# Optimization experiments

Measured on AMD Instinct MI355X. Metric: run time of the kernel, lower is better.

Reference implementation:

```python
import jax, jax.numpy as jnp
import numpy as np

B, H, W, C, HID, V, EMB = 16, 24, 96, 1024, 256, 5000, 256
BN_EPS = 1e-5


def _lin(k, fin, fout, s=0.05):
    return jax.random.normal(k, (fin, fout), jnp.float32) * s


def setup_inputs():
    ks = jax.random.split(jax.random.key(0), 24)
    inp = {
        "input_y": jax.random.randint(ks[0], (B,), 0, V),
        "input_hidden": jax.random.normal(ks[1], (B, 1, HID), jnp.float32),
        "img_feature": jax.random.normal(ks[2], (B, C, H, W), jnp.float32),
        "feature_w": W,
        "attention_sum": jnp.zeros((B, 1, H, W), jnp.float32),
        "alpha_t": jax.random.uniform(ks[3], (B, 1, H, W), jnp.float32),
        "feature_h": H,
        "batch_size": B,
        "h_mask": jax.random.randint(ks[4], (B,), 1, H + 1),
        "w_mask": jax.random.randint(ks[5], (B,), 1, W + 1),
        "emb_table": jax.random.normal(ks[6], (V, EMB), jnp.float32) * 0.05,
        "gru1_wi": _lin(ks[7], EMB, 3 * HID), "gru1_wh": _lin(ks[8], HID, 3 * HID),
        "gru1_bi": jnp.zeros((3 * HID,), jnp.float32), "gru1_bh": jnp.zeros((3 * HID,), jnp.float32),
        "fc1_w": _lin(ks[9], HID, 256), "fc1_b": jnp.zeros((256,), jnp.float32),
        "gru2_wi": _lin(ks[10], C, 3 * HID), "gru2_wh": _lin(ks[11], HID, 3 * HID),
        "gru2_bi": jnp.zeros((3 * HID,), jnp.float32), "gru2_bh": jnp.zeros((3 * HID,), jnp.float32),
        "out_w": _lin(ks[12], 128, V), "out_b": jnp.zeros((V,), jnp.float32),
        "emb2_w": _lin(ks[13], 256, 128), "emb2_b": jnp.zeros((128,), jnp.float32),
        "conv1_w": jax.random.normal(ks[14], (1, 1, 3, 3), jnp.float32) * 0.05,
        "conv1_b": jnp.zeros((1,), jnp.float32),
        "conv_tan_w": jax.random.normal(ks[15], (256, 256, 3, 3), jnp.float32) * 0.02,
        "conv_tan_b": jnp.zeros((256,), jnp.float32),
        "fc2_w": _lin(ks[16], HID, 128), "fc2_b": jnp.zeros((128,), jnp.float32),
        "ua_w": _lin(ks[17], C, 256), "ua_b": jnp.zeros((256,), jnp.float32),
        "uf_w": _lin(ks[18], 1, 256), "uf_b": jnp.zeros((256,), jnp.float32),
        "v_w": _lin(ks[19], 256, 1), "v_b": jnp.zeros((1,), jnp.float32),
        "wc_w": _lin(ks[20], C, 128), "wc_b": jnp.zeros((128,), jnp.float32),
        "bn1_gamma": jnp.ones((256,), jnp.float32), "bn1_beta": jnp.zeros((256,), jnp.float32),
        "bn1_mean": jnp.zeros((256,), jnp.float32), "bn1_var": jnp.ones((256,), jnp.float32),
    }
    return inp


def _gru(x, h, wi, wh, bi, bh):
    # PyTorch GRUCell semantics
    gi = x @ wi + bi
    gh = h @ wh + bh
    ir, iz, inn = jnp.split(gi, 3, axis=-1)
    hr, hz, hn = jnp.split(gh, 3, axis=-1)
    r = jax.nn.sigmoid(ir + hr)
    z = jax.nn.sigmoid(iz + hz)
    n = jnp.tanh(inn + r * hn)
    return (1.0 - z) * n + z * h


def _conv(x, w, b):
    y = jax.lax.conv_general_dilated(x, w, (1, 1), 'SAME',
                                     dimension_numbers=('NCHW', 'OIHW', 'NCHW'))
    return y + b[None, :, None, None]


def reference(input_y, input_hidden, img_feature, feature_w, attention_sum, alpha_t,
              feature_h, batch_size, h_mask, w_mask,
              emb_table, gru1_wi, gru1_wh, gru1_bi, gru1_bh, fc1_w, fc1_b,
              gru2_wi, gru2_wh, gru2_bi, gru2_bh, out_w, out_b, emb2_w, emb2_b,
              conv1_w, conv1_b, conv_tan_w, conv_tan_b, fc2_w, fc2_b,
              ua_w, ua_b, uf_w, uf_b, v_w, v_b, wc_w, wc_b,
              bn1_gamma, bn1_beta, bn1_mean, bn1_var):
    b, c, h, w = img_feature.shape
    # per-sample validity mask over the feature map  [B, H, W]
    et_mask = ((jnp.arange(h)[None, :] < h_mask[:, None])[:, :, None]
               & (jnp.arange(w)[None, :] < w_mask[:, None])[:, None, :]).astype(jnp.float32)

    emb = emb_table[input_y]                      # [B, 256] (dropout = identity, eval)
    h0 = input_hidden[:, 0, :]                    # [B, HID]
    st1 = _gru(emb, h0, gru1_wi, gru1_wh, gru1_bi, gru1_bh)
    st1 = st1 @ fc1_w + fc1_b                     # [B, 256]

    alpha_c = _conv(alpha_t, conv1_w, conv1_b)    # [B, 1, H, W]
    att_sum = attention_sum + alpha_c             # coverage accumulator

    img1 = jnp.einsum('bchw,cd->bhwd', img_feature, ua_w) + ua_b  # [B,H,W,256]
    att1 = att_sum[:, 0, :, :, None] * uf_w[0] + uf_b             # Linear(1,256)
    et = st1[:, None, None, :] + img1 + att1      # [B, H, W, 256]

    et_nchw = jnp.transpose(et, (0, 3, 1, 2))
    et_nchw = _conv(et_nchw, conv_tan_w, conv_tan_b)
    et_nchw = et_nchw * et_mask[:, None]
    inv = bn1_gamma / jnp.sqrt(bn1_var + BN_EPS)  # eval-mode BatchNorm2d(256)
    et_nchw = (et_nchw - bn1_mean[None, :, None, None]) * inv[None, :, None, None] \
              + bn1_beta[None, :, None, None]
    et_nchw = jnp.tanh(et_nchw)

    e = jnp.einsum('bchw,c->bhw', et_nchw, v_w[:, 0]) + v_b[0]    # [B, H, W]
    e_exp = jnp.exp(e) * et_mask
    e_sum = jnp.sum(e_exp, axis=(1, 2))
    alpha = e_exp / (e_sum[:, None, None] + 1e-8)                 # masked softmax

    ct = jnp.einsum('bhw,bchw->bc', alpha, img_feature)           # [B, 1024]
    st = _gru(ct, st1, gru2_wi, gru2_wh, gru2_bi, gru2_bh)        # [B, HID]
    hidden_next = st[:, None, :]

    pre = (st @ fc2_w + fc2_b) + (emb @ emb2_w + emb2_b) + (ct @ wc_w + wc_b)  # [B,128]
    output = jax.nn.log_softmax(pre @ out_w + out_b, axis=1)[:, None, :]       # [B,1,V]
    return output, hidden_next, alpha[:, None], att_sum
```

## Files before the change

### kernel.cpp

```cpp
#include <hip/hip_runtime.h>
#include <hip/hip_bf16.h>

#define B   16
#define H   24
#define W   96
#define C   1024
#define HID 256
#define V   5000
#define EMB 256
#define HW  (H*W)
#define BN_EPS 1e-5f
#define H2  (H+2)
#define W2  (W+2)

#define OUT0 0
#define OUT1 (B*V)
#define OUT2 (OUT1 + B*HID)
#define OUT3 (OUT2 + B*HW)

#define WSB_IMGT  0
#define WSB_ETP   75497472
#define WSB_WTB   96370688
#define WSB_UAT   97550336
#define WSB_E     98074624
#define WSB_ST1   98369536
#define WSB_CT    98385920
#define WSB_PRE   98451456
#define WSB_GIGH1 98459648
#define WSB_GH2   98574336
#define WSB_GI2   98631680

typedef __attribute__((ext_vector_type(8))) short short8;
typedef __attribute__((ext_vector_type(4))) float f32x4;

__device__ inline unsigned short f2bf(float f) {
    union { float f; unsigned int u; } v; v.f = f;
    unsigned int r = v.u + 0x7fffu + ((v.u >> 16) & 1u);
    return (unsigned short)(r >> 16);
}
__device__ inline float bf2f(unsigned short u) {
    union { unsigned int u; float f; } v; v.u = ((unsigned int)u) << 16;
    return v.f;
}

__global__ __launch_bounds__(256) void k_imgT(const float* img, unsigned short* imgT)
{
    int hw0 = blockIdx.x*64, c0 = blockIdx.y*128, b = blockIdx.z;
    int t = threadIdx.x;
    __shared__ __align__(16) unsigned short tr[64*256];
    int row = t & 63;
    int sgb = t >> 6;
    const float* src = img + ((size_t)b*C + c0)*HW + hw0 + row;
    #pragma unroll
    for (int k = 0; k < 4; ++k) {
        int sg = sgb + k*4;
        union { short8 v; unsigned short u[8]; } pk;
        #pragma unroll
        for (int j = 0; j < 8; ++j)
            pk.u[j] = f2bf(src[(size_t)(sg*8 + j)*HW]);
        *(short8*)&tr[row*256 + (sg ^ (row & 31))*8] = pk.v;
    }
    __syncthreads();
    #pragma unroll
    for (int k = 0; k < 4; ++k) {
        int i = k*256 + t;
        int orow = i >> 4, sg = i & 15;
        *(short8*)&imgT[((size_t)(b*HW) + hw0 + orow)*1024 + c0 + sg*8] =
            *(const short8*)&tr[orow*256 + (sg ^ (orow & 31))*8];
    }
}

__global__ __launch_bounds__(256) void k_prep(
    const float* conv_w_src, unsigned short* wtb,
    const float* ua_w, unsigned short* uat,
    const float* att_in, const float* alpha_t, const float* cw, const float* cb, float* att_out,
    float* ct, unsigned short* et_p)
{
    int x = blockIdx.x, t = threadIdx.x;
    if (x < 2304) {
        int idx = x*256 + t;
        int c = idx & 255; int o = (idx >> 8) & 255; int khw = idx >> 16;
        wtb[(khw*256 + o)*256 + c] = f2bf(conv_w_src[(o*256 + c)*9 + khw]);
    } else if (x < 3328) {
        int idx = (x - 2304)*256 + t;
        int c = idx & 1023; int d = idx >> 10;
        uat[d*1024 + c] = f2bf(ua_w[c*256 + d]);
    } else if (x < 3472) {
        int i = (x - 3328)*256 + t;
        int w = i % W; int h = (i / W) % H; int b = i / HW;
        float s = cb[0];
        #pragma unroll
        for (int kh = 0; kh < 3; ++kh) {
            int r = h + kh - 1; if (r < 0 || r >= H) continue;
            #pragma unroll
            for (int kw = 0; kw < 3; ++kw) {
                int c = w + kw - 1; if (c < 0 || c >= W) continue;
                s += alpha_t[(b*H + r)*W + c]*cw[kh*3+kw];
            }
        }
        att_out[i] = att_in[i] + s;
    } else if (x < 3536) {
        ct[(x - 3472)*256 + t] = 0.f;
    } else {
        int flat = (x - 3536)*256 + t;
        int b = flat / 7808; int r = flat - b*7808;
        int h2, w2, j;
        if (r < 3136)      { h2 = 0;  w2 = r >> 5;          j = r & 31; }
        else if (r < 6272) { h2 = 25; w2 = (r - 3136) >> 5; j = (r - 3136) & 31; }
        else {
            int rr = r - 6272;
            h2 = 1 + (rr >> 6);
            int s = rr & 63;
            w2 = (s < 32) ? 0 : 97;
            j = s & 31;
        }
        ((int4*)et_p)[((size_t)(b*H2 + h2)*W2 + w2)*32 + j] = make_int4(0,0,0,0);
    }
}

__global__ __launch_bounds__(256) void k_tail1(
    const int* y, const float* emb_table, const float* h0,
    const float* wi, const float* wh, float* gigh)
{
    int virt = blockIdx.x*16;
    int t = threadIdx.x;
    bool gi_mode = virt < 768;
    __shared__ float a_l[16*256];
    for (int i = t; i < 4096; i += 256) {
        int b = i >> 8, k = i & 255;
        a_l[i] = gi_mode ? emb_table[y[b]*EMB + k] : h0[b*HID + k];
    }
    __syncthreads();
    int nl = t & 15, b = t >> 4;
    int n = (gi_mode ? virt : virt - 768) + nl;
    const float* wp = gi_mode ? wi : wh;
    float acc = 0.f;
    #pragma unroll 16
    for (int k = 0; k < 256; ++k) acc += a_l[b*256 + k]*wp[k*768 + n];
    gigh[b*1536 + virt + nl] = acc;
}

__global__ __launch_bounds__(256) void k_fc1c(
    const float* gigh, const float* h0, const float* bi, const float* bh,
    const float* fc1_w, const float* fc1_b, float* st1)
{
    int n0 = blockIdx.x*16, t = threadIdx.x;
    __shared__ float a_l[16*256];
    for (int i = t; i < 4096; i += 256) {
        int b = i >> 8, k = i & 255;
        const float* g = gigh + b*1536;
        float ir = g[k] + bi[k], iz = g[256+k] + bi[256+k], in_ = g[512+k] + bi[512+k];
        float hr = g[768+k] + bh[k], hz = g[1024+k] + bh[256+k], hn = g[1280+k] + bh[512+k];
        float r = 1.f/(1.f+__expf(-(ir+hr)));
        float z = 1.f/(1.f+__expf(-(iz+hz)));
        float n = tanhf(in_ + r*hn);
        a_l[i] = (1.f - z)*n + z*h0[b*HID + k];
    }
    __syncthreads();
    int nl = t & 15, b = t >> 4;
    float acc = fc1_b[n0+nl];
    #pragma unroll 16
    for (int k = 0; k < 256; ++k) acc += a_l[b*256+k]*fc1_w[k*256 + n0 + nl];
    st1[b*256 + n0 + nl] = acc;
}

__global__ __launch_bounds__(256, 3) void k_et(
    const unsigned short* imgT, const unsigned short* uat, const float* ua_b,
    const float* st1, const float* att_sum, const float* uf_w, const float* uf_b,
    unsigned short* et_p)
{
    int h = blockIdx.x, ny = blockIdx.y, b = blockIdx.z;
    int t = threadIdx.x;
    int wv = t >> 6, lane = t & 63, q = lane >> 4, ln = lane & 15;
    int wm = wv & 1, wn = wv >> 1;
    int n0 = ny*128 + wn*64;
    __shared__ __align__(16) unsigned short a_l[96*256];

    f32x4 acc[12];
    #pragma unroll
    for (int i = 0; i < 12; ++i) acc[i] = (f32x4){0.f,0.f,0.f,0.f};

    const unsigned short* ab = imgT + ((size_t)(b*HW) + h*W)*1024;
    const unsigned short* bbase = uat + (size_t)(n0 + ln)*1024 + q*8;

    int slot0 = q ^ (ln & 7);
    int ebase[3];
    #pragma unroll
    for (int mf = 0; mf < 3; ++mf)
        ebase[mf] = (wm*48 + ln + 16*mf)*256 + slot0*8;

    for (int c0 = 0; c0 < 1024; c0 += 128) {
        __syncthreads();
        #pragma unroll
        for (int k = 0; k < 6; ++k) {
            int i = t + k*256;
            int m = i >> 4, sg = i & 15;
            ((int4*)a_l)[m*32 + ((sg & 8) | ((sg ^ m) & 7))] =
                *((const int4*)(ab + (size_t)m*1024 + c0) + sg);
        }
        __syncthreads();
        #pragma unroll
        for (int cs = 0; cs < 128; cs += 32) {
            short8 av[3];
            #pragma unroll
            for (int mf = 0; mf < 3; ++mf)
                av[mf] = *(const short8*)&a_l[ebase[mf] ^ cs];
            #pragma unroll
            for (int j = 0; j < 4; ++j) {
                short8 bv = *(const short8*)(bbase + (size_t)(j*16)*1024 + c0 + cs);
                #pragma unroll
                for (int mf = 0; mf < 3; ++mf)
                    acc[mf*4+j] = __builtin_amdgcn_mfma_f32_16x16x32_bf16(av[mf], bv, acc[mf*4+j], 0, 0, 0);
            }
        }
    }

    float att_m[12];
    #pragma unroll
    for (int mf = 0; mf < 3; ++mf)
        #pragma unroll
        for (int r = 0; r < 4; ++r)
            att_m[mf*4+r] = att_sum[(b*H + h)*W + wm*48 + mf*16 + q*4 + r];
    #pragma unroll
    for (int j = 0; j < 4; ++j) {
        int n = n0 + j*16 + ln;
        float s1 = st1[b*256 + n] + ua_b[n];
        float ufw = uf_w[n], ufb = uf_b[n];
        #pragma unroll
        for (int mf = 0; mf < 3; ++mf)
            #pragma unroll
            for (int r = 0; r < 4; ++r) {
                int m = wm*48 + mf*16 + q*4 + r;
                float v = acc[mf*4+j][r] + s1 + att_m[mf*4+r]*ufw + ufb;
                et_p[((size_t)(b*H2 + h + 1)*W2 + (m + 1))*256 + n] = f2bf(v);
            }
    }
}

__global__ __launch_bounds__(256, 3) void k_conv(
    const unsigned short* et_p, const unsigned short* wtb, const float* cb,
    const float* bn_g, const float* bn_b, const float* bn_m, const float* bn_v,
    const float* v_w, float* e_part)
{
    int h = blockIdx.x, ny = blockIdx.y, b = blockIdx.z;
    int t = threadIdx.x;
    int wv = t >> 6, lane = t & 63, q = lane >> 4, ln = lane & 15;
    int wm = wv & 1, wn = wv >> 1;
    int n0 = ny*128 + wn*64;
    __shared__ __align__(16) unsigned short patch[3*6400];
    __shared__ float lds_red[2][96];

    f32x4 acc[12];
    #pragma unroll
    for (int i = 0; i < 12; ++i) acc[i] = (f32x4){0.f,0.f,0.f,0.f};

    int abase[3][3];
    #pragma unroll
    for (int mf = 0; mf < 3; ++mf)
        #pragma unroll
        for (int kw = 0; kw < 3; ++kw) {
            int x2 = wm*48 + ln + 16*mf + kw;
            int sp0 = ((x2 & 3) << 3) | ((q ^ (x2 & 7)) & 7);
            abase[mf][kw] = (x2 >> 2)*256 + sp0*8;
        }

    const int4* ebase_g = (const int4*)et_p;

    for (int c0 = 0; c0 < 256; c0 += 64) {
        __syncthreads();
        for (int i = t; i < 2352; i += 256) {
            int kh = i / 784; int r = i - kh*784; int x2 = r >> 3; int sg = r & 7;
            int sp = ((x2 & 3) << 3) | ((sg ^ (x2 & 7)) & 7);
            ((int4*)patch)[kh*800 + (x2 >> 2)*32 + sp] =
                ebase_g[((size_t)(b*H2 + h + kh)*W2 + x2)*32 + (c0 >> 3) + sg];
        }
        __syncthreads();
        #pragma unroll
        for (int kh = 0; kh < 3; ++kh) {
            #pragma unroll
            for (int kw = 0; kw < 3; ++kw) {
                const unsigned short* brow = wtb + ((size_t)((kh*3 + kw)*256 + n0 + ln))*256 + c0 + q*8;
                #pragma unroll
                for (int cs = 0; cs < 64; cs += 32) {
                    short8 av[3];
                    #pragma unroll
                    for (int mf = 0; mf < 3; ++mf)
                        av[mf] = *(const short8*)&patch[kh*6400 + (abase[mf][kw] ^ cs)];
                    #pragma unroll
                    for (int j = 0; j < 4; ++j) {
                        short8 bv = *(const short8*)(brow + j*4096 + cs);
                        #pragma unroll
                        for (int mf = 0; mf < 3; ++mf)
                            acc[mf*4+j] = __builtin_amdgcn_mfma_f32_16x16x32_bf16(av[mf], bv, acc[mf*4+j], 0, 0, 0);
                    }
                }
            }
        }
    }

    float psum[12];
    #pragma unroll
    for (int i = 0; i < 12; ++i) psum[i] = 0.f;
    #pragma unroll
    for (int j = 0; j < 4; ++j) {
        int o = n0 + j*16 + ln;
        float inv  = bn_g[o]*rsqrtf(bn_v[o] + BN_EPS);
        float mean = bn_m[o], beta = bn_b[o], bias = cb[o], vw = v_w[o];
        #pragma unroll
        for (int mf = 0; mf < 3; ++mf)
            #pragma unroll
            for (int r = 0; r < 4; ++r) {
                float x = (acc[mf*4+j][r] + bias - mean)*inv + beta;
                x = fminf(fmaxf(x, -15.f), 15.f);
                float ex = __expf(2.f*x);
                psum[mf*4+r] += ((ex - 1.f)/(ex + 1.f))*vw;
            }
    }
    #pragma unroll
    for (int s = 1; s < 16; s <<= 1)
        #pragma unroll
        for (int i = 0; i < 12; ++i) psum[i] += __shfl_xor(psum[i], s);
    if (ln == 0) {
        #pragma unroll
        for (int mf = 0; mf < 3; ++mf)
            #pragma unroll
            for (int r = 0; r < 4; ++r)
                lds_red[wn][wm*48 + mf*16 + q*4 + r] = psum[mf*4+r];
    }
    __syncthreads();
    if (t < 96)
        e_part[(size_t)ny*(B*HW) + (b*H + h)*W + t] = lds_red[0][t] + lds_red[1][t];
}

__global__ __launch_bounds__(256) void k_softmax(
    const float* e_part, const int* h_mask, const int* w_mask, const float* v_b,
    float* alpha_out)
{
    int b = blockIdx.x, t = threadIdx.x;
    int hm = h_mask[b], wm = w_mask[b];
    float vb = v_b[0];
    __shared__ float red[256];
    float vals[9];
    float loc = 0.f;
    #pragma unroll
    for (int i = 0; i < 9; ++i) {
        int hw = t + i*256;
        int hh = hw / W, ww = hw % W;
        float v = 0.f;
        if (hh < hm && ww < wm)
            v = __expf(e_part[b*HW + hw] + e_part[B*HW + b*HW + hw] + vb);
        vals[i] = v; loc += v;
    }
    red[t] = loc; __syncthreads();
    for (int s = 128; s > 0; s >>= 1) { if (t < s) red[t] += red[t+s]; __syncthreads(); }
    float inv = 1.f/(red[0] + 1e-8f);
    #pragma unroll
    for (int i = 0; i < 9; ++i) alpha_out[b*HW + t + i*256] = vals[i]*inv;
}

__global__ __launch_bounds__(256) void k_ct(
    const float* alpha, const unsigned short* imgT, float* ct)
{
    int s = blockIdx.x, b = blockIdx.y, t = threadIdx.x;
    int cg = (t & 127)*8, half = t >> 7;
    float acc[8];
    #pragma unroll
    for (int j = 0; j < 8; ++j) acc[j] = 0.f;
    for (int i = 0; i < 72; ++i) {
        int hw = s*144 + i*2 + half;
        float a = alpha[b*HW + hw];
        union { short8 v; unsigned short u[8]; } pk;
        pk.v = *(const short8*)&imgT[((size_t)(b*HW) + hw)*1024 + cg];
        #pragma unroll
        for (int j = 0; j < 8; ++j) acc[j] += a*bf2f(pk.u[j]);
    }
    #pragma unroll
    for (int j = 0; j < 8; ++j) atomicAdd(&ct[b*1024 + cg + j], acc[j]);
}

__global__ __launch_bounds__(256) void k_g2(
    const float* st1, const int* y, const float* emb_table,
    const float* wh, const float* emb2_w, float* gh2,
    const float* ct, const float* wi, const float* wc_w, float* gi2p)
{
    int x = blockIdx.x, t = threadIdx.x;
    __shared__ float a_l[16*256];
    if (x < 56) {
        int virt = x*16;
        bool ghm = virt < 768;
        for (int i = t; i < 4096; i += 256) {
            int b = i >> 8, k = i & 255;
            a_l[i] = ghm ? st1[b*256 + k] : emb_table[y[b]*EMB + k];
        }
        __syncthreads();
        int nl = t & 15, b = t >> 4;
        float acc = 0.f;
        if (ghm) {
            int n = virt + nl;
            #pragma unroll 16
            for (int k = 0; k < 256; ++k) acc += a_l[b*256+k]*wh[k*768 + n];
        } else {
            int n = virt - 768 + nl;
            #pragma unroll 16
            for (int k = 0; k < 256; ++k) acc += a_l[b*256+k]*emb2_w[k*128 + n];
        }
        gh2[b*896 + virt + nl] = acc;
    } else {
        int xx = x - 56;
        int ks = xx / 56, virt = (xx - ks*56)*16;
        int k0 = ks*256;
        for (int i = t; i < 4096; i += 256) {
            int b = i >> 8, k = i & 255;
            a_l[i] = ct[b*1024 + k0 + k];
        }
        __syncthreads();
        int nl = t & 15, b = t >> 4;
        float acc = 0.f;
        if (virt < 768) {
            int n = virt + nl;
            #pragma unroll 16
            for (int k = 0; k < 256; ++k) acc += a_l[b*256+k]*wi[(k0+k)*768 + n];
        } else {
            int n = virt - 768 + nl;
            #pragma unroll 16
            for (int k = 0; k < 256; ++k) acc += a_l[b*256+k]*wc_w[(k0+k)*128 + n];
        }
        gi2p[(ks*16 + b)*896 + virt + nl] = acc;
    }
}

__global__ __launch_bounds__(256) void k_fc2c(
    const float* gi2p, const float* gh2, const float* st1,
    const float* bi, const float* bh,
    const float* fc2_w, const float* fc2_b, const float* emb2_b, const float* wc_b,
    float* hidden_out, float* pre)
{
    int n0 = blockIdx.x*16, t = threadIdx.x;
    __shared__ float st_l[16*256];
    for (int i = t; i < 4096; i += 256) {
        int b = i >> 8, k = i & 255;
        float ir = bi[k], iz = bi[256+k], in_ = bi[512+k];
        #pragma unroll
        for (int ks = 0; ks < 4; ++ks) {
            const float* g = gi2p + (ks*16 + b)*896;
            ir += g[k]; iz += g[256+k]; in_ += g[512+k];
        }
        const float* gh = gh2 + b*896;
        float hr = gh[k] + bh[k], hz = gh[256+k] + bh[256+k], hn = gh[512+k] + bh[512+k];
        float h = st1[b*256+k];
        float r = 1.f/(1.f+__expf(-(ir+hr)));
        float z = 1.f/(1.f+__expf(-(iz+hz)));
        float n = tanhf(in_ + r*hn);
        float s = (1.f - z)*n + z*h;
        st_l[i] = s;
        if (blockIdx.x == 0) hidden_out[b*HID + k] = s;
    }
    __syncthreads();
    int nl = t & 15, b = t >> 4;
    int n = n0 + nl;
    float acc = fc2_b[n] + emb2_b[n] + wc_b[n] + gh2[b*896 + 768 + n];
    #pragma unroll
    for (int ks = 0; ks < 4; ++ks) acc += gi2p[(ks*16 + b)*896 + 768 + n];
    #pragma unroll 16
    for (int k = 0; k < 256; ++k) acc += st_l[b*256+k]*fc2_w[k*128 + n];
    pre[b*128 + n] = acc;
}

__global__ __launch_bounds__(256) void k_logits(
    const float* pre, const float* out_w, const float* out_b, float* out)
{
    int j0 = blockIdx.x*64, t = threadIdx.x;
    __shared__ float pre_l[16*128];
    for (int i = t; i < 2048; i += 256) pre_l[i] = pre[i];
    __syncthreads();
    int jl = t & 63, bg = t >> 6;
    int j = j0 + jl;
    if (j >= V) return;
    float acc0=0.f, acc1=0.f, acc2=0.f, acc3=0.f;
    const float* pl = pre_l + bg*4*128;
    #pragma unroll 8
    for (int k = 0; k < 128; ++k) {
        float wv = out_w[k*V + j];
        acc0 += pl[k]*wv; acc1 += pl[128+k]*wv; acc2 += pl[256+k]*wv; acc3 += pl[384+k]*wv;
    }
    float ob = out_b[j];
    out[(bg*4+0)*V + j] = acc0 + ob;
    out[(bg*4+1)*V + j] = acc1 + ob;
    out[(bg*4+2)*V + j] = acc2 + ob;
    out[(bg*4+3)*V + j] = acc3 + ob;
}

__global__ __launch_bounds__(1024) void k_lsm(float* out)
{
    int b = blockIdx.x, t = threadIdx.x;
    __shared__ float red[1024];
    float lg[5]; float mx = -1e30f;
    #pragma unroll
    for (int i = 0; i < 5; ++i) {
        int j = t + i*1024;
        lg[i] = (j < V) ? out[b*V + j] : -1e30f;
        mx = fmaxf(mx, lg[i]);
    }
    red[t] = mx; __syncthreads();
    for (int s = 512; s > 0; s >>= 1) { if (t < s) red[t] = fmaxf(red[t], red[t+s]); __syncthreads(); }
    float gmax = red[0]; __syncthreads();
    float se = 0.f;
    #pragma unroll
    for (int i = 0; i < 5; ++i) { int j = t + i*1024; if (j < V) se += __expf(lg[i] - gmax); }
    red[t] = se; __syncthreads();
    for (int s = 512; s > 0; s >>= 1) { if (t < s) red[t] += red[t+s]; __syncthreads(); }
    float lse = logf(red[0]);
    #pragma unroll
    for (int i = 0; i < 5; ++i) { int j = t + i*1024; if (j < V) out[b*V + j] = lg[i] - gmax - lse; }
}

extern "C" void kernel_launch(void* const* d_in, const int* in_sizes, int n_in,
                              void* d_out, int out_size, void* d_ws, size_t ws_size,
                              hipStream_t stream)
{
    const int*   input_y      = (const int*)  d_in[0];
    const float* input_hidden = (const float*)d_in[1];
    const float* img          = (const float*)d_in[2];
    const float* attention    = (const float*)d_in[4];
    const float* alpha_t      = (const float*)d_in[5];
    const int*   h_mask       = (const int*)  d_in[8];
    const int*   w_mask       = (const int*)  d_in[9];
    const float* emb_table    = (const float*)d_in[10];
    const float* gru1_wi      = (const float*)d_in[11];
    const float* gru1_wh      = (const float*)d_in[12];
    const float* gru1_bi      = (const float*)d_in[13];
    const float* gru1_bh      = (const float*)d_in[14];
    const float* fc1_w        = (const float*)d_in[15];
    const float* fc1_b        = (const float*)d_in[16];
    const float* gru2_wi      = (const float*)d_in[17];
    const float* gru2_wh      = (const float*)d_in[18];
    const float* gru2_bi      = (const float*)d_in[19];
    const float* gru2_bh      = (const float*)d_in[20];
    const float* out_w        = (const float*)d_in[21];
    const float* out_b        = (const float*)d_in[22];
    const float* emb2_w       = (const float*)d_in[23];
    const float* emb2_b       = (const float*)d_in[24];
    const float* conv1_w      = (const float*)d_in[25];
    const float* conv1_b      = (const float*)d_in[26];
    const float* conv_tan_w   = (const float*)d_in[27];
    const float* conv_tan_b   = (const float*)d_in[28];
    const float* fc2_w        = (const float*)d_in[29];
    const float* fc2_b        = (const float*)d_in[30];
    const float* ua_w         = (const float*)d_in[31];
    const float* ua_b         = (const float*)d_in[32];
    const float* uf_w         = (const float*)d_in[33];
    const float* uf_b         = (const float*)d_in[34];
    const float* v_w          = (const float*)d_in[35];
    const float* v_b          = (const float*)d_in[36];
    const float* wc_w         = (const float*)d_in[37];
    const float* wc_b         = (const float*)d_in[38];
    const float* bn1_gamma    = (const float*)d_in[39];
    const float* bn1_beta     = (const float*)d_in[40];
    const float* bn1_mean     = (const float*)d_in[41];
    const float* bn1_var      = (const float*)d_in[42];

    float* out = (float*)d_out;
    char*  ws  = (char*)d_ws;
    unsigned short* imgT = (unsigned short*)(ws + WSB_IMGT);
    unsigned short* et_p = (unsigned short*)(ws + WSB_ETP);
    unsigned short* wtb  = (unsigned short*)(ws + WSB_WTB);
    unsigned short* uat  = (unsigned short*)(ws + WSB_UAT);
    float* e_part = (float*)(ws + WSB_E);
    float* st1   = (float*)(ws + WSB_ST1);
    float* ct    = (float*)(ws + WSB_CT);
    float* pre   = (float*)(ws + WSB_PRE);
    float* gigh1 = (float*)(ws + WSB_GIGH1);
    float* gh2   = (float*)(ws + WSB_GH2);
    float* gi2p  = (float*)(ws + WSB_GI2);

    float* out_logits = out + OUT0;
    float* out_hidden = out + OUT1;
    float* out_alpha  = out + OUT2;
    float* out_attsum = out + OUT3;

    k_imgT<<<dim3(HW/64, C/128, B), 256, 0, stream>>>(img, imgT);
    k_prep<<<4024, 256, 0, stream>>>(conv_tan_w, wtb, ua_w, uat,
                                     attention, alpha_t, conv1_w, conv1_b, out_attsum,
                                     ct, et_p);
    k_tail1<<<96, 256, 0, stream>>>(input_y, emb_table, input_hidden,
                                    gru1_wi, gru1_wh, gigh1);
    k_fc1c<<<16, 256, 0, stream>>>(gigh1, input_hidden, gru1_bi, gru1_bh,
                                   fc1_w, fc1_b, st1);
    k_et<<<dim3(H, 2, B), 256, 0, stream>>>(imgT, uat, ua_b, st1, out_attsum,
                                            uf_w, uf_b, et_p);
    k_conv<<<dim3(H, 2, B), 256, 0, stream>>>(et_p, wtb, conv_tan_b,
                                              bn1_gamma, bn1_beta, bn1_mean, bn1_var,
                                              v_w, e_part);
    k_softmax<<<B, 256, 0, stream>>>(e_part, h_mask, w_mask, v_b, out_alpha);
    k_ct<<<dim3(16, B), 256, 0, stream>>>(out_alpha, imgT, ct);
    k_g2<<<280, 256, 0, stream>>>(st1, input_y, emb_table, gru2_wh, emb2_w, gh2,
                                  ct, gru2_wi, wc_w, gi2p);
    k_fc2c<<<8, 256, 0, stream>>>(gi2p, gh2, st1, gru2_bi, gru2_bh,
                                  fc2_w, fc2_b, emb2_b, wc_b, out_hidden, pre);
    k_logits<<<(V + 63)/64, 256, 0, stream>>>(pre, out_w, out_b, out_logits);
    k_lsm<<<B, 1024, 0, stream>>>(out_logits);
}
```

Baseline: 610.2 us.

## Double-buffer LDS tiles via direct global-to-LDS loads in k_et and k_conv

Replaces the register-staged global-to-shared copies in the et-projection GEMM and the 3x3 conv kernel with direct global_load_lds transfers into two alternating LDS buffers. The next channel chunk is prefetched while MFMAs run on the current one, and one barrier per iteration replaces two. The swizzle now moves from the LDS write side to the global read side, and the conv chunk shrinks to 32 channels. The aim is to hide global load latency and cut VGPR use for staging, at the cost of more iterations, smaller LDS tiles, and reliance on the LDS layout being correct for the lane-contiguous writes.

```diff
diff --git a/kernel.cpp b/kernel.cpp
--- a/kernel.cpp
+++ b/kernel.cpp
@@ -41,6 +41,13 @@
 __device__ inline float bf2f(unsigned short u) {
     union { unsigned int u; float f; } v; v.u = ((unsigned int)u) << 16;
     return v.f;
+}
+
+__device__ inline void gload_lds16(const unsigned short* g, unsigned short* l) {
+    __builtin_amdgcn_global_load_lds(
+        (const __attribute__((address_space(1))) void*)g,
+        (__attribute__((address_space(3))) void*)l,
+        16, 0, 0);
 }
 
 __global__ __launch_bounds__(256) void k_imgT(const float* img, unsigned short* imgT)
@@ -174,7 +181,7 @@
     int wv = t >> 6, lane = t & 63, q = lane >> 4, ln = lane & 15;
     int wm = wv & 1, wn = wv >> 1;
     int n0 = ny*128 + wn*64;
-    __shared__ __align__(16) unsigned short a_l[96*256];
+    __shared__ __align__(16) unsigned short a_l[2*1536*8];
 
     f32x4 acc[12];
     #pragma unroll
@@ -183,28 +190,41 @@
     const unsigned short* ab = imgT + ((size_t)(b*HW) + h*W)*1024;
     const unsigned short* bbase = uat + (size_t)(n0 + ln)*1024 + q*8;
 
-    int slot0 = q ^ (ln & 7);
     int ebase[3];
     #pragma unroll
-    for (int mf = 0; mf < 3; ++mf)
-        ebase[mf] = (wm*48 + ln + 16*mf)*256 + slot0*8;
-
+    for (int mf = 0; mf < 3; ++mf) {
+        int m = wm*48 + ln + 16*mf;
+        ebase[mf] = m*128 + (q ^ (m & 7))*8;
+    }
+
+    int goff[6], loff[6];
+    #pragma unroll
+    for (int it = 0; it < 6; ++it) {
+        int L = it*256 + t;
+        int m = L >> 4, s = L & 15;
+        goff[it] = m*1024 + (s ^ (m & 7))*8;
+        loff[it] = (it*256 + wv*64)*8;
+    }
+
+    #pragma unroll
+    for (int it = 0; it < 6; ++it)
+        gload_lds16(ab + goff[it], &a_l[loff[it]]);
+    __syncthreads();
+
+    int cur = 0;
     for (int c0 = 0; c0 < 1024; c0 += 128) {
-        __syncthreads();
-        #pragma unroll
-        for (int k = 0; k < 6; ++k) {
-            int i = t + k*256;
-            int m = i >> 4, sg = i & 15;
-            ((int4*)a_l)[m*32 + ((sg & 8) | ((sg ^ m) & 7))] =
-                *((const int4*)(ab + (size_t)m*1024 + c0) + sg);
-        }
-        __syncthreads();
+        int bufS = cur*12288, nbufS = bufS ^ 12288;
+        if (c0 < 896) {
+            #pragma unroll
+            for (int it = 0; it < 6; ++it)
+                gload_lds16(ab + goff[it] + c0 + 128, &a_l[nbufS + loff[it]]);
+        }
         #pragma unroll
         for (int cs = 0; cs < 128; cs += 32) {
             short8 av[3];
             #pragma unroll
             for (int mf = 0; mf < 3; ++mf)
-                av[mf] = *(const short8*)&a_l[ebase[mf] ^ cs];
+                av[mf] = *(const short8*)&a_l[bufS + (ebase[mf] ^ cs)];
             #pragma unroll
             for (int j = 0; j < 4; ++j) {
                 short8 bv = *(const short8*)(bbase + (size_t)(j*16)*1024 + c0 + cs);
@@ -213,6 +233,8 @@
                     acc[mf*4+j] = __builtin_amdgcn_mfma_f32_16x16x32_bf16(av[mf], bv, acc[mf*4+j], 0, 0, 0);
             }
         }
+        __syncthreads();
+        cur ^= 1;
     }
 
     float att_m[12];
@@ -247,7 +269,7 @@
     int wv = t >> 6, lane = t & 63, q = lane >> 4, ln = lane & 15;
     int wm = wv & 1, wn = wv >> 1;
     int n0 = ny*128 + wn*64;
-    __shared__ __align__(16) unsigned short patch[3*6400];
+    __shared__ __align__(16) unsigned short patch[2*1176*8];
     __shared__ float lds_red[2][96];
 
     f32x4 acc[12];
@@ -260,42 +282,59 @@
         #pragma unroll
         for (int kw = 0; kw < 3; ++kw) {
             int x2 = wm*48 + ln + 16*mf + kw;
-            int sp0 = ((x2 & 3) << 3) | ((q ^ (x2 & 7)) & 7);
-            abase[mf][kw] = (x2 >> 2)*256 + sp0*8;
-        }
-
-    const int4* ebase_g = (const int4*)et_p;
-
-    for (int c0 = 0; c0 < 256; c0 += 64) {
-        __syncthreads();
-        for (int i = t; i < 2352; i += 256) {
-            int kh = i / 784; int r = i - kh*784; int x2 = r >> 3; int sg = r & 7;
-            int sp = ((x2 & 3) << 3) | ((sg ^ (x2 & 7)) & 7);
-            ((int4*)patch)[kh*800 + (x2 >> 2)*32 + sp] =
-                ebase_g[((size_t)(b*H2 + h + kh)*W2 + x2)*32 + (c0 >> 3) + sg];
-        }
-        __syncthreads();
+            abase[mf][kw] = x2*32 + (q ^ ((x2 >> 1) & 3))*8;
+        }
+
+    const unsigned short* gb = et_p + (size_t)(b*H2 + h)*W2*256;
+    const unsigned short* wb = wtb + (size_t)(n0 + ln)*256 + q*8;
+
+    int goff[5], loff[5]; bool act[5];
+    #pragma unroll
+    for (int it = 0; it < 5; ++it) {
+        int L = it*256 + t;
+        act[it] = L < 1176;
+        int Lc = act[it] ? L : 0;
+        int pl = Lc / 392; int rem = Lc - pl*392;
+        int x2 = rem >> 2, s = rem & 3;
+        goff[it] = (pl*W2 + x2)*256 + (s ^ ((x2 >> 1) & 3))*8;
+        loff[it] = (it*256 + wv*64)*8;
+    }
+
+    #pragma unroll
+    for (int it = 0; it < 5; ++it)
+        if (act[it]) gload_lds16(gb + goff[it], &patch[loff[it]]);
+    __syncthreads();
+
+    int cur = 0;
+    for (int cc = 0; cc < 8; ++cc) {
+        int bufS = cur*9408, nbufS = bufS ^ 9408;
+        if (cc < 7) {
+            int c1 = (cc + 1)*32;
+            #pragma unroll
+            for (int it = 0; it < 5; ++it)
+                if (act[it]) gload_lds16(gb + goff[it] + c1, &patch[nbufS + loff[it]]);
+        }
+        int c0 = cc*32;
         #pragma unroll
         for (int kh = 0; kh < 3; ++kh) {
             #pragma unroll
             for (int kw = 0; kw < 3; ++kw) {
-                const unsigned short* brow = wtb + ((size_t)((kh*3 + kw)*256 + n0 + ln))*256 + c0 + q*8;
+                short8 av[3];
                 #pragma unroll
-                for (int cs = 0; cs < 64; cs += 32) {
-                    short8 av[3];
+                for (int mf = 0; mf < 3; ++mf)
+                    av[mf] = *(const short8*)&patch[bufS + kh*3136 + abase[mf][kw]];
+                const unsigned short* brow = wb + (size_t)(kh*3 + kw)*65536 + c0;
+                #pragma unroll
+                for (int j = 0; j < 4; ++j) {
+                    short8 bv = *(const short8*)(brow + j*4096);
                     #pragma unroll
                     for (int mf = 0; mf < 3; ++mf)
-                        av[mf] = *(const short8*)&patch[kh*6400 + (abase[mf][kw] ^ cs)];
-                    #pragma unroll
-                    for (int j = 0; j < 4; ++j) {
-                        short8 bv = *(const short8*)(brow + j*4096 + cs);
-                        #pragma unroll
-                        for (int mf = 0; mf < 3; ++mf)
-                            acc[mf*4+j] = __builtin_amdgcn_mfma_f32_16x16x32_bf16(av[mf], bv, acc[mf*4+j], 0, 0, 0);
-                    }
+                        acc[mf*4+j] = __builtin_amdgcn_mfma_f32_16x16x32_bf16(av[mf], bv, acc[mf*4+j], 0, 0, 0);
                 }
             }
         }
+        __syncthreads();
+        cur ^= 1;
     }
 
     float psum[12];
```

Result: no change. 604.6 us (-0.9%).

## Repack weight matrices into k-chunk-major layout and move LDS swizzle to global reads

Applied to the files above, without the earlier changes.

Both the conv and ua weights are now packed as [k/8][n][8] in bf16, so the 16 lanes of a B fragment read consecutive 16-byte chunks and the loads coalesce instead of striding by 1024 or 256 elements. The LDS tiles in k_et and k_conv drop the padded and interleaved layout for a plain row layout, with the XOR swizzle applied to the global source index. This shrinks shared memory in both kernels, which may allow more blocks per CU. The cross-warp reduction buffer in k_conv is reindexed to match.

```diff
diff --git a/kernel.cpp b/kernel.cpp
--- a/kernel.cpp
+++ b/kernel.cpp
@@ -80,11 +80,12 @@
     if (x < 2304) {
         int idx = x*256 + t;
         int c = idx & 255; int o = (idx >> 8) & 255; int khw = idx >> 16;
-        wtb[(khw*256 + o)*256 + c] = f2bf(conv_w_src[(o*256 + c)*9 + khw]);
+        wtb[(((size_t)khw*32 + (c >> 3))*256 + o)*8 + (c & 7)] =
+            f2bf(conv_w_src[(o*256 + c)*9 + khw]);
     } else if (x < 3328) {
         int idx = (x - 2304)*256 + t;
         int c = idx & 1023; int d = idx >> 10;
-        uat[d*1024 + c] = f2bf(ua_w[c*256 + d]);
+        uat[((size_t)(c >> 3)*256 + d)*8 + (c & 7)] = f2bf(ua_w[c*256 + d]);
     } else if (x < 3472) {
         int i = (x - 3328)*256 + t;
         int w = i % W; int h = (i / W) % H; int b = i / HW;
@@ -174,29 +175,29 @@
     int wv = t >> 6, lane = t & 63, q = lane >> 4, ln = lane & 15;
     int wm = wv & 1, wn = wv >> 1;
     int n0 = ny*128 + wn*64;
-    __shared__ __align__(16) unsigned short a_l[96*256];
+    __shared__ __align__(16) unsigned short a_l[96*128];
 
     f32x4 acc[12];
     #pragma unroll
     for (int i = 0; i < 12; ++i) acc[i] = (f32x4){0.f,0.f,0.f,0.f};
 
     const unsigned short* ab = imgT + ((size_t)(b*HW) + h*W)*1024;
-    const unsigned short* bbase = uat + (size_t)(n0 + ln)*1024 + q*8;
-
-    int slot0 = q ^ (ln & 7);
+
     int ebase[3];
     #pragma unroll
-    for (int mf = 0; mf < 3; ++mf)
-        ebase[mf] = (wm*48 + ln + 16*mf)*256 + slot0*8;
+    for (int mf = 0; mf < 3; ++mf) {
+        int m = wm*48 + ln + 16*mf;
+        ebase[mf] = m*128 + (q ^ (m & 7))*8;
+    }
 
     for (int c0 = 0; c0 < 1024; c0 += 128) {
         __syncthreads();
         #pragma unroll
         for (int k = 0; k < 6; ++k) {
             int i = t + k*256;
-            int m = i >> 4, sg = i & 15;
-            ((int4*)a_l)[m*32 + ((sg & 8) | ((sg ^ m) & 7))] =
-                *((const int4*)(ab + (size_t)m*1024 + c0) + sg);
+            int m = i >> 4, s = i & 15;
+            ((int4*)a_l)[m*16 + s] =
+                *((const int4*)(ab + (size_t)m*1024 + c0) + (s ^ (m & 7)));
         }
         __syncthreads();
         #pragma unroll
@@ -205,9 +206,11 @@
             #pragma unroll
             for (int mf = 0; mf < 3; ++mf)
                 av[mf] = *(const short8*)&a_l[ebase[mf] ^ cs];
+            const unsigned short* bp =
+                uat + ((size_t)(((c0 + cs) >> 3) + q)*256 + n0 + ln)*8;
             #pragma unroll
             for (int j = 0; j < 4; ++j) {
-                short8 bv = *(const short8*)(bbase + (size_t)(j*16)*1024 + c0 + cs);
+                short8 bv = *(const short8*)(bp + j*128);
                 #pragma unroll
                 for (int mf = 0; mf < 3; ++mf)
                     acc[mf*4+j] = __builtin_amdgcn_mfma_f32_16x16x32_bf16(av[mf], bv, acc[mf*4+j], 0, 0, 0);
@@ -247,8 +250,8 @@
     int wv = t >> 6, lane = t & 63, q = lane >> 4, ln = lane & 15;
     int wm = wv & 1, wn = wv >> 1;
     int n0 = ny*128 + wn*64;
-    __shared__ __align__(16) unsigned short patch[3*6400];
-    __shared__ float lds_red[2][96];
+    __shared__ __align__(16) unsigned short patch[3*98*64];
+    __shared__ float lds_red[4][48];
 
     f32x4 acc[12];
     #pragma unroll
@@ -260,35 +263,35 @@
         #pragma unroll
         for (int kw = 0; kw < 3; ++kw) {
             int x2 = wm*48 + ln + 16*mf + kw;
-            int sp0 = ((x2 & 3) << 3) | ((q ^ (x2 & 7)) & 7);
-            abase[mf][kw] = (x2 >> 2)*256 + sp0*8;
-        }
-
-    const int4* ebase_g = (const int4*)et_p;
+            abase[mf][kw] = x2*64 + (q ^ (x2 & 7))*8;
+        }
+
+    const int4* gsrc = (const int4*)et_p;
 
     for (int c0 = 0; c0 < 256; c0 += 64) {
         __syncthreads();
         for (int i = t; i < 2352; i += 256) {
-            int kh = i / 784; int r = i - kh*784; int x2 = r >> 3; int sg = r & 7;
-            int sp = ((x2 & 3) << 3) | ((sg ^ (x2 & 7)) & 7);
-            ((int4*)patch)[kh*800 + (x2 >> 2)*32 + sp] =
-                ebase_g[((size_t)(b*H2 + h + kh)*W2 + x2)*32 + (c0 >> 3) + sg];
+            int kh = i / 784; int r = i - kh*784; int x2 = r >> 3; int s = r & 7;
+            ((int4*)patch)[kh*784 + x2*8 + s] =
+                gsrc[((size_t)(b*H2 + h + kh)*W2 + x2)*32 + (c0 >> 3) + (s ^ (x2 & 7))];
         }
         __syncthreads();
         #pragma unroll
         for (int kh = 0; kh < 3; ++kh) {
             #pragma unroll
             for (int kw = 0; kw < 3; ++kw) {
-                const unsigned short* brow = wtb + ((size_t)((kh*3 + kw)*256 + n0 + ln))*256 + c0 + q*8;
                 #pragma unroll
                 for (int cs = 0; cs < 64; cs += 32) {
                     short8 av[3];
                     #pragma unroll
                     for (int mf = 0; mf < 3; ++mf)
-                        av[mf] = *(const short8*)&patch[kh*6400 + (abase[mf][kw] ^ cs)];
+                        av[mf] = *(const short8*)&patch[kh*6272 + (abase[mf][kw] ^ cs)];
+                    const unsigned short* bp = wtb
+                        + (size_t)(kh*3 + kw)*65536
+                        + ((size_t)(((c0 + cs) >> 3) + q)*256 + n0 + ln)*8;
                     #pragma unroll
                     for (int j = 0; j < 4; ++j) {
-                        short8 bv = *(const short8*)(brow + j*4096 + cs);
+                        short8 bv = *(const short8*)(bp + j*128);
                         #pragma unroll
                         for (int mf = 0; mf < 3; ++mf)
                             acc[mf*4+j] = __builtin_amdgcn_mfma_f32_16x16x32_bf16(av[mf], bv, acc[mf*4+j], 0, 0, 0);
@@ -325,11 +328,14 @@
         for (int mf = 0; mf < 3; ++mf)
             #pragma unroll
             for (int r = 0; r < 4; ++r)
-                lds_red[wn][wm*48 + mf*16 + q*4 + r] = psum[mf*4+r];
+                lds_red[wv][mf*16 + q*4 + r] = psum[mf*4+r];
     }
     __syncthreads();
-    if (t < 96)
-        e_part[(size_t)ny*(B*HW) + (b*H + h)*W + t] = lds_red[0][t] + lds_red[1][t];
+    if (t < 96) {
+        int wmr = t / 48, lr = t - wmr*48;
+        e_part[(size_t)ny*(B*HW) + (b*H + h)*W + t] =
+            lds_red[wmr][lr] + lds_red[wmr + 2][lr];
+    }
 }
 
 __global__ __launch_bounds__(256) void k_softmax(
```

New measurement: 598.1 us. 2.0% less time.
